# Kernel optimization log

Measured on AMD Instinct MI355X. Metric: run time of the kernel, lower is better.

The kernel has to match this reference:

```python
import jax, jax.numpy as jnp
import numpy as np

P = 16        # patch size
SIM = 0.3     # similarity threshold (forward default arg `sim`)
STY_STD = 1000.0


def patchify(imgs):
    # (N,3,H,W) -> (N, h*w, p*p*3)
    N, C, H, W = imgs.shape
    h, w = H // P, W // P
    x = imgs.reshape(N, C, h, P, w, P)
    x = jnp.einsum('nchpwq->nhwpqc', x)
    return x.reshape(N, h * w, P * P * C)


def setup_inputs() -> dict:
    key = jax.random.key(0)
    k1, k2, k3, k4 = jax.random.split(key, 4)
    N, L, D = 2, 196, 768
    x = jax.random.normal(k1, (N, L + 1, D), dtype=jnp.float32)
    imgs = jax.random.normal(k2, (N, 3, 224, 224), dtype=jnp.float32)
    # torch trunc_normal_(std=1000, a=-2, b=2) == truncated normal on [-2,2]
    learnable_sty = (jax.random.truncated_normal(
        k3, -2.0 / STY_STD, 2.0 / STY_STD, (N, L, L, 1), dtype=jnp.float32) * STY_STD)
    noise = jax.random.normal(k4, (N, L, L, 1), dtype=jnp.float32)
    return {"x": x, "imgs": imgs, "learnable_sty": learnable_sty, "noise": noise}


def reference(x, imgs, learnable_sty, noise):
    imgs = patchify(imgs)                                   # (N, L, 768)
    cls_tokens, x = x[:, :1], x[:, 1:]
    N, L, D = x.shape

    # per-patch normalization (torch.var default is unbiased -> ddof=1)
    mean = imgs.mean(axis=-1, keepdims=True)
    var = jnp.var(imgs, axis=-1, keepdims=True, ddof=1)
    imgs_n = (imgs - mean) / jnp.sqrt(var + 1e-6)
    nrm = jnp.linalg.norm(imgs_n, axis=-1)                  # (N, L)
    Sim = jnp.einsum('aik,ajk->aij', imgs_n, imgs_n) / (nrm[:, :, None] * nrm[:, None, :])

    M0 = jnp.triu((Sim > SIM).astype(jnp.float32))          # (N, L, L), binary
    rows = jnp.arange(L)

    def body(i, M):
        # original loop breaks when sum == N*L; we freeze M once that holds
        done = M.sum() == N * L
        mask = (M[:, i, :] == 0).astype(M.dtype)            # (N, L)
        # rows <= i unchanged (M*M == M for binary), rows > i masked
        upd = jnp.where(rows[None, :, None] > i, M * mask[:, None, :], M)
        return jnp.where(done, M, upd)

    M = jax.lax.fori_loop(0, L - 1, body, M0)

    # decompose: phase (con) keeps grad, amplitude (sty) is detached
    fft = jnp.fft.fftn(x, axes=(-1,))
    con, sty = jnp.angle(fft), jnp.abs(fft)
    sty_d = jax.lax.stop_gradient(sty)

    avg_sum = (M[..., None] * sty_d[:, None, :, :]).sum(axis=2)   # (N, L, D)
    sty_mask = (avg_sum > 0).astype(jnp.float32)                   # (N, L, D)
    num = M.sum(axis=2)[..., None]                                 # (N, L, 1)
    avg = avg_sum / jnp.clip(num, 1e-7, None)                      # (N, L, D)
    std = jnp.sqrt(
        (M[..., None] * (sty_d[:, None, :, :] - avg[:, :, None, :]) ** 2).sum(axis=2)
        / jnp.clip(num, 1e-7, None))                               # (N, L, D)

    sty_para = sty_mask[:, None, :, :] * learnable_sty             # (N, L, L, D)
    sty_para = sty_para / jnp.clip(sty_para.sum(axis=2, keepdims=True), 1e-7, None)
    various = noise * std[:, None, :, :] + avg[:, None, :, :]      # (N, L, L, D)
    sum_sty = (sty_para * various).sum(axis=2)                     # (N, L, D)

    # compose: ifft(amp * e^{i phase}), torch .float() keeps the real part
    out = jnp.real(jnp.fft.ifftn(sum_sty * jnp.exp(1j * con), axes=(-1,))).astype(jnp.float32)
    return jnp.concatenate((cls_tokens, out), axis=1)
```

## Files before the change

### kernel.cpp

```cpp
#include <hip/hip_runtime.h>
#include <math.h>

typedef unsigned long long u64;

#define NBATCH 2
#define LTOK 196
#define DDIM 768
#define NROWS (NBATCH*LTOK)
#define NLD (NBATCH*LTOK*DDIM)

#ifndef M_PI
#define M_PI 3.14159265358979323846
#endif
#define PI_F 3.14159265358979323846f

#define S3 0.86602540378443864676f

__device__ __forceinline__ void fft_butterfly(float* re, float* im,
                                              const float2* T,
                                              int tau, int s, int half) {
  int sub = tau >> 7;
  int b = tau & 127;
  int j = b & (half - 1);
  int p0 = (sub << 8) + ((b >> (s - 1)) << s) + j;
  int p1 = p0 + half;
  float2 w = T[j << (8 - s)];
  float xr = re[p1], xi = im[p1];
  float tr = w.x * xr - w.y * xi;
  float ti = w.x * xi + w.y * xr;
  float ur = re[p0], ui = im[p0];
  re[p0] = ur + tr; im[p0] = ui + ti;
  re[p1] = ur - tr; im[p1] = ui - ti;
}

__device__ __forceinline__ void fft_stages(float* re, float* im,
                                           const float2* T, int t) {
#pragma unroll
  for (int s = 1; s <= 8; s++) {
    int half = 1 << (s - 1);
    fft_butterfly(re, im, T, t, s, half);
    if (t < 128) fft_butterfly(re, im, T, t + 256, s, half);
    __syncthreads();
  }
}

__global__ __launch_bounds__(256) void k_pre(const float* __restrict__ imgs,
                                             const float* __restrict__ x,
                                             float* __restrict__ uT,
                                             float* __restrict__ sty,
                                             float* __restrict__ phre,
                                             float* __restrict__ phim) {
  int t = threadIdx.x;
  if (blockIdx.x < NROWS) {
    int blk = blockIdx.x;
    int a = blk / LTOK, l = blk - a * LTOK;
    int hh = l / 14, ww = l - hh * 14;
    float loc[3];
    double s = 0.0, sq = 0.0;
#pragma unroll
    for (int e = 0; e < 3; e++) {
      int d = t + (e << 8);
      int p = d / 48, r = d - p * 48;
      int q2 = r / 3, c = r - q2 * 3;
      float val = imgs[((size_t)(a * 3 + c) * 224 + (hh * 16 + p)) * 224 + (ww * 16 + q2)];
      loc[e] = val;
      s += (double)val;
      sq += (double)val * (double)val;
    }
#pragma unroll
    for (int o = 32; o > 0; o >>= 1) { s += __shfl_down(s, o); sq += __shfl_down(sq, o); }
    __shared__ double rs[4], rq[4];
    __shared__ float sh_mu, sh_sc;
    if ((t & 63) == 0) { rs[t >> 6] = s; rq[t >> 6] = sq; }
    __syncthreads();
    if (t == 0) {
      double S = rs[0] + rs[1] + rs[2] + rs[3];
      double Q = rq[0] + rq[1] + rq[2] + rq[3];
      double mean = S / 768.0;
      double ss = Q - S * S / 768.0;
      if (ss < 1e-30) ss = 1e-30;
      sh_mu = (float)mean;
      sh_sc = (float)(1.0 / sqrt(ss));
    }
    __syncthreads();
    float mu = sh_mu, sc = sh_sc;
    int col = a * LTOK + l;
#pragma unroll
    for (int e = 0; e < 3; e++) {
      int d = t + (e << 8);
      uT[(size_t)d * NROWS + col] = (loc[e] - mu) * sc;
    }
  } else {
    int blk = blockIdx.x - NROWS;
    int a = blk / LTOK, i = blk - a * LTOK;
    __shared__ float re[768], im[768];
    __shared__ float2 t256[128];
    if (t < 128) {
      float sn, cs;
      __sincosf(-2.0f * PI_F * (float)t / 256.0f, &sn, &cs);
      t256[t] = make_float2(cs, sn);
    }
    size_t row = ((size_t)a * (LTOK + 1) + 1 + i) * DDIM;
#pragma unroll
    for (int e = 0; e < 3; e++) {
      int d = t + (e << 8);
      int m = d / 3, r = d - 3 * m;
      int p = (r << 8) + (__brev((unsigned)m) >> 24);
      re[p] = x[row + d];
      im[p] = 0.f;
    }
    __syncthreads();
    fft_stages(re, im, t256, t);
    float a0r = re[t],       a0i = im[t];
    float a1r = re[256 + t], a1i = im[256 + t];
    float a2r = re[512 + t], a2i = im[512 + t];
    float sn, cs;
    __sincosf(-2.0f * PI_F * (float)t / 768.0f, &sn, &cs);
    float2 w1 = make_float2(cs, sn);
    float2 w2 = make_float2(cs * cs - sn * sn, 2.f * cs * sn);
    float b1r = a1r * w1.x - a1i * w1.y, b1i = a1r * w1.y + a1i * w1.x;
    float b2r = a2r * w2.x - a2i * w2.y, b2i = a2r * w2.y + a2i * w2.x;
    float Xr[3], Xi[3];
    Xr[0] = a0r + b1r + b2r;
    Xi[0] = a0i + b1i + b2i;
    Xr[1] = a0r + (-0.5f * b1r + S3 * b1i) + (-0.5f * b2r - S3 * b2i);
    Xi[1] = a0i + (-0.5f * b1i - S3 * b1r) + (-0.5f * b2i + S3 * b2r);
    Xr[2] = a0r + (-0.5f * b1r - S3 * b1i) + (-0.5f * b2r + S3 * b2i);
    Xi[2] = a0i + (-0.5f * b1i + S3 * b1r) + (-0.5f * b2i - S3 * b2r);
    size_t ob = ((size_t)a * LTOK + i) * DDIM + t;
#pragma unroll
    for (int s = 0; s < 3; s++) {
      float mag = sqrtf(Xr[s] * Xr[s] + Xi[s] * Xi[s]);
      size_t o = ob + (s << 8);
      sty[o] = mag;
      if (mag > 0.f) { phre[o] = Xr[s] / mag; phim[o] = Xi[s] / mag; }
      else           { phre[o] = 1.f;         phim[o] = 0.f;         }
    }
  }
}

__global__ __launch_bounds__(256) void k_sim(const float* __restrict__ uT,
                                             u64* __restrict__ Mb) {
  int blk = blockIdx.x;
  int a = blk / LTOK, i = blk - a * LTOK;
  __shared__ float ui[768];
  __shared__ u64 mask[4];
  int t = threadIdx.x;
  if (t < 4) mask[t] = 0ull;
  int coli = a * LTOK + i;
#pragma unroll
  for (int e = 0; e < 3; e++) {
    int d = t + (e << 8);
    ui[d] = uT[(size_t)d * NROWS + coli];
  }
  __syncthreads();
  int j = i + t;
  if (j < LTOK) {
    const float* col = uT + (a * LTOK + j);
    float dot = 0.f;
#pragma unroll 8
    for (int d = 0; d < 768; d++) dot += ui[d] * col[(size_t)d * NROWS];
    if (dot > 0.3f) atomicOr(&mask[j >> 6], 1ull << (j & 63));
  }
  __syncthreads();
  if (t < 4) Mb[((size_t)a * LTOK + i) * 4 + t] = mask[t];
}

__global__ __launch_bounds__(256) void k_greedy(u64* __restrict__ Mb) {
  __shared__ u64 Ml[NROWS * 4];
  __shared__ int red[4];
  __shared__ int Sdone;
  int t = threadIdx.x;
  for (int w = t; w < NROWS * 4; w += 256) Ml[w] = Mb[w];
  __syncthreads();
  for (int i = 0; i < LTOK - 1; i++) {
    int s = 0;
    for (int w = t; w < NROWS * 4; w += 256) s += __popcll(Ml[w]);
#pragma unroll
    for (int o = 32; o > 0; o >>= 1) s += __shfl_down(s, o);
    if ((t & 63) == 0) red[t >> 6] = s;
    __syncthreads();
    if (t == 0) Sdone = ((red[0] + red[1] + red[2] + red[3]) == NROWS) ? 1 : 0;
    __syncthreads();
    if (Sdone) break;
    for (int w = t; w < NROWS * 4; w += 256) {
      int a = w / (LTOK * 4);
      int rem = w - a * (LTOK * 4);
      int r = rem >> 2, wi = rem & 3;
      if (r > i) Ml[w] &= ~Ml[(a * LTOK + i) * 4 + wi];
    }
    __syncthreads();
  }
  for (int w = t; w < NROWS * 4; w += 256) Mb[w] = Ml[w];
}

__global__ __launch_bounds__(256) void k_stats(const u64* __restrict__ Mb,
                                               const float* __restrict__ sty,
                                               float* __restrict__ savg,
                                               float* __restrict__ sstd,
                                               float* __restrict__ smsk) {
  int blk = blockIdx.x;
  int a = blk / LTOK, i = blk - a * LTOK;
  __shared__ u64 mrow[4];
  int t = threadIdx.x;
  if (t < 4) mrow[t] = Mb[((size_t)a * LTOK + i) * 4 + t];
  __syncthreads();
  int num = __popcll(mrow[0]) + __popcll(mrow[1]) + __popcll(mrow[2]) + __popcll(mrow[3]);
  float fnum = fmaxf((float)num, 1e-7f);
  float acc0 = 0.f, acc1 = 0.f, acc2 = 0.f;
  for (int w = 0; w < 4; w++) {
    u64 m = mrow[w];
    while (m) {
      int b = __ffsll(m) - 1; m &= (m - 1);
      int j = (w << 6) + b;
      const float* sr = sty + ((size_t)a * LTOK + j) * DDIM;
      acc0 += sr[t]; acc1 += sr[t + 256]; acc2 += sr[t + 512];
    }
  }
  float av0 = acc0 / fnum, av1 = acc1 / fnum, av2 = acc2 / fnum;
  float sq0 = 0.f, sq1 = 0.f, sq2 = 0.f;
  for (int w = 0; w < 4; w++) {
    u64 m = mrow[w];
    while (m) {
      int b = __ffsll(m) - 1; m &= (m - 1);
      int j = (w << 6) + b;
      const float* sr = sty + ((size_t)a * LTOK + j) * DDIM;
      float d0 = sr[t] - av0, d1 = sr[t + 256] - av1, d2 = sr[t + 512] - av2;
      sq0 += d0 * d0; sq1 += d1 * d1; sq2 += d2 * d2;
    }
  }
  size_t o = ((size_t)a * LTOK + i) * DDIM + t;
  float mk0 = acc0 > 0.f ? 1.f : 0.f;
  float mk1 = acc1 > 0.f ? 1.f : 0.f;
  float mk2 = acc2 > 0.f ? 1.f : 0.f;
  smsk[o] = mk0;            smsk[o + 256] = mk1;            smsk[o + 512] = mk2;
  savg[o] = mk0 * av0;      savg[o + 256] = mk1 * av1;      savg[o + 512] = mk2 * av2;
  sstd[o] = mk0 * sqrtf(sq0 / fnum);
  sstd[o + 256] = mk1 * sqrtf(sq1 / fnum);
  sstd[o + 512] = mk2 * sqrtf(sq2 / fnum);
}

#define RTILE 7
__global__ __launch_bounds__(256) void k_combine(const float* __restrict__ ls,
                                                 const float* __restrict__ nz,
                                                 const float* __restrict__ savg,
                                                 const float* __restrict__ sstd,
                                                 const float* __restrict__ smsk,
                                                 float* __restrict__ ssum) {
  int blk = blockIdx.x;
  int a = blk / 84;
  int rem = blk - a * 84;
  int it = rem / 3, dc = rem - it * 3;
  int i0 = it * RTILE;
  int t = threadIdx.x;
  int d = (dc << 8) + t;
  __shared__ float lsr[RTILE][LTOK], lnr[RTILE][LTOK];
  for (int idx = t; idx < RTILE * LTOK; idx += 256) {
    int ii = idx / LTOK, j = idx - ii * LTOK;
    size_t o = ((size_t)(a * LTOK + i0 + ii)) * LTOK + j;
    float l = ls[o];
    lsr[ii][j] = l;
    lnr[ii][j] = l * nz[o];
  }
  __syncthreads();
  float a1[RTILE], a2[RTILE], dn[RTILE];
#pragma unroll
  for (int ii = 0; ii < RTILE; ii++) { a1[ii] = 0.f; a2[ii] = 0.f; dn[ii] = 0.f; }
#pragma unroll 2
  for (int j = 0; j < LTOK; j++) {
    size_t b = ((size_t)a * LTOK + j) * DDIM + d;
    float sd = sstd[b], sv = savg[b], sm = smsk[b];
#pragma unroll
    for (int ii = 0; ii < RTILE; ii++) {
      a1[ii] += lnr[ii][j] * sd;
      a2[ii] += lsr[ii][j] * sv;
      dn[ii] += lsr[ii][j] * sm;
    }
  }
#pragma unroll
  for (int ii = 0; ii < RTILE; ii++) {
    size_t o = ((size_t)(a * LTOK + i0 + ii)) * DDIM + d;
    ssum[o] = (a1[ii] + a2[ii]) / fmaxf(dn[ii], 1e-7f);
  }
}

__global__ __launch_bounds__(256) void k_ifft(const float* __restrict__ x,
                                              const float* __restrict__ ssum,
                                              const float* __restrict__ phre,
                                              const float* __restrict__ phim,
                                              float* __restrict__ out) {
  int blk = blockIdx.x;
  int t = threadIdx.x;
  if (blk < NBATCH) {
    size_t b = (size_t)blk * (LTOK + 1) * DDIM;
    out[b + t] = x[b + t];
    out[b + t + 256] = x[b + t + 256];
    out[b + t + 512] = x[b + t + 512];
    return;
  }
  int rr = blk - NBATCH;
  int a = rr / LTOK, i = rr - a * LTOK;
  __shared__ float re[768], im[768];
  __shared__ float2 t256[128];
  if (t < 128) {
    float sn, cs;
    __sincosf(2.0f * PI_F * (float)t / 256.0f, &sn, &cs);
    t256[t] = make_float2(cs, sn);
  }
  size_t rowz = ((size_t)a * LTOK + i) * DDIM;
#pragma unroll
  for (int e = 0; e < 3; e++) {
    int d = t + (e << 8);
    int m = d / 3, r = d - 3 * m;
    int p = (r << 8) + (__brev((unsigned)m) >> 24);
    float mg = ssum[rowz + d];
    re[p] = mg * phre[rowz + d];
    im[p] = mg * phim[rowz + d];
  }
  __syncthreads();
  fft_stages(re, im, t256, t);
  float a0r = re[t],       a0i = im[t];
  float a1r = re[256 + t], a1i = im[256 + t];
  float a2r = re[512 + t], a2i = im[512 + t];
  float sn, cs;
  __sincosf(2.0f * PI_F * (float)t / 768.0f, &sn, &cs);
  float2 w1 = make_float2(cs, sn);
  float2 w2 = make_float2(cs * cs - sn * sn, 2.f * cs * sn);
  float b1r = a1r * w1.x - a1i * w1.y, b1i = a1r * w1.y + a1i * w1.x;
  float b2r = a2r * w2.x - a2i * w2.y, b2i = a2r * w2.y + a2i * w2.x;
  float Xr[3];
  Xr[0] = a0r + b1r + b2r;
  Xr[1] = a0r + (-0.5f * b1r - S3 * b1i) + (-0.5f * b2r + S3 * b2i);
  Xr[2] = a0r + (-0.5f * b1r + S3 * b1i) + (-0.5f * b2r - S3 * b2i);
  size_t ob = ((size_t)a * (LTOK + 1) + 1 + i) * DDIM + t;
  const float inv = 1.0f / 768.0f;
  out[ob]       = Xr[0] * inv;
  out[ob + 256] = Xr[1] * inv;
  out[ob + 512] = Xr[2] * inv;
}

extern "C" void kernel_launch(void* const* d_in, const int* in_sizes, int n_in,
                              void* d_out, int out_size, void* d_ws, size_t ws_size,
                              hipStream_t stream) {
  (void)in_sizes; (void)n_in; (void)out_size; (void)ws_size;
  const float* x    = (const float*)d_in[0];
  const float* imgs = (const float*)d_in[1];
  const float* ls   = (const float*)d_in[2];
  const float* nz   = (const float*)d_in[3];
  float* out = (float*)d_out;

  float* wf   = (float*)d_ws;
  float* uT   = wf;
  float* sty  = wf + (size_t)NLD;
  float* phre = wf + 2 * (size_t)NLD;
  float* phim = wf + 3 * (size_t)NLD;
  float* sstd = wf + 4 * (size_t)NLD;
  float* smsk = wf + 5 * (size_t)NLD;
  u64* Mb = (u64*)(wf + 6 * (size_t)NLD);

  k_pre    <<<2 * NROWS, 256, 0, stream>>>(imgs, x, uT, sty, phre, phim);
  k_sim    <<<NROWS, 256, 0, stream>>>(uT, Mb);
  k_greedy <<<1, 256, 0, stream>>>(Mb);
  k_stats  <<<NROWS, 256, 0, stream>>>(Mb, sty, uT , sstd, smsk);
  k_combine<<<NBATCH * 28 * 3, 256, 0, stream>>>(ls, nz, uT , sstd, smsk, sty );
  k_ifft   <<<NBATCH + NROWS, 256, 0, stream>>>(x, sty , phre, phim, out);
}
```

Measured before the change: 145.5 us.

## Split combine reduction over j into four chunks, reduce partials in ifft

The combine kernel's loop over the 196 source tokens is split into four chunks of 49, which raises the block count from 168 to 672 so the GPU's compute units are better filled. Partial numerators and denominators are written to new workspace buffers, and the ifft kernel sums the four partials before dividing. This adds extra global writes and reads of partial sums and a larger workspace footprint in exchange for more parallelism. The two numerator accumulators are also merged into one.

Result: faster. 125.4 us (-13.8%).

```diff
diff --git a/kernel.cpp b/kernel.cpp
--- a/kernel.cpp
+++ b/kernel.cpp
@@ -9,11 +9,7 @@
 #define NROWS (NBATCH*LTOK)
 #define NLD (NBATCH*LTOK*DDIM)
 
-#ifndef M_PI
-#define M_PI 3.14159265358979323846
-#endif
 #define PI_F 3.14159265358979323846f
-
 #define S3 0.86602540378443864676f
 
 __device__ __forceinline__ void fft_butterfly(float* re, float* im,
@@ -241,51 +237,60 @@
 }
 
 #define RTILE 7
-__global__ __launch_bounds__(256) void k_combine(const float* __restrict__ ls,
-                                                 const float* __restrict__ nz,
-                                                 const float* __restrict__ savg,
-                                                 const float* __restrict__ sstd,
-                                                 const float* __restrict__ smsk,
-                                                 float* __restrict__ ssum) {
+#define JCH 4
+#define JLEN 49
+__global__ __launch_bounds__(256) void k_combine_part(const float* __restrict__ ls,
+                                                      const float* __restrict__ nz,
+                                                      const float* __restrict__ savg,
+                                                      const float* __restrict__ sstd,
+                                                      const float* __restrict__ smsk,
+                                                      float* __restrict__ numP,
+                                                      float* __restrict__ denP) {
   int blk = blockIdx.x;
-  int a = blk / 84;
-  int rem = blk - a * 84;
-  int it = rem / 3, dc = rem - it * 3;
+  int a = blk / 336;
+  int rem = blk - a * 336;
+  int it = rem / 12;
+  int r2 = rem - it * 12;
+  int dc = r2 >> 2;
+  int jc = r2 & 3;
   int i0 = it * RTILE;
+  int j0 = jc * JLEN;
   int t = threadIdx.x;
   int d = (dc << 8) + t;
-  __shared__ float lsr[RTILE][LTOK], lnr[RTILE][LTOK];
-  for (int idx = t; idx < RTILE * LTOK; idx += 256) {
-    int ii = idx / LTOK, j = idx - ii * LTOK;
-    size_t o = ((size_t)(a * LTOK + i0 + ii)) * LTOK + j;
+  __shared__ float lsr[RTILE][JLEN], lnr[RTILE][JLEN];
+  for (int idx = t; idx < RTILE * JLEN; idx += 256) {
+    int ii = idx / JLEN, j = idx - ii * JLEN;
+    size_t o = ((size_t)(a * LTOK + i0 + ii)) * LTOK + j0 + j;
     float l = ls[o];
     lsr[ii][j] = l;
     lnr[ii][j] = l * nz[o];
   }
   __syncthreads();
-  float a1[RTILE], a2[RTILE], dn[RTILE];
-#pragma unroll
-  for (int ii = 0; ii < RTILE; ii++) { a1[ii] = 0.f; a2[ii] = 0.f; dn[ii] = 0.f; }
-#pragma unroll 2
-  for (int j = 0; j < LTOK; j++) {
-    size_t b = ((size_t)a * LTOK + j) * DDIM + d;
+  float nm[RTILE], dn[RTILE];
+#pragma unroll
+  for (int ii = 0; ii < RTILE; ii++) { nm[ii] = 0.f; dn[ii] = 0.f; }
+#pragma unroll 7
+  for (int j = 0; j < JLEN; j++) {
+    size_t b = ((size_t)(a * LTOK + j0 + j)) * DDIM + d;
     float sd = sstd[b], sv = savg[b], sm = smsk[b];
 #pragma unroll
     for (int ii = 0; ii < RTILE; ii++) {
-      a1[ii] += lnr[ii][j] * sd;
-      a2[ii] += lsr[ii][j] * sv;
+      nm[ii] += lnr[ii][j] * sd;
+      nm[ii] += lsr[ii][j] * sv;
       dn[ii] += lsr[ii][j] * sm;
     }
   }
 #pragma unroll
   for (int ii = 0; ii < RTILE; ii++) {
-    size_t o = ((size_t)(a * LTOK + i0 + ii)) * DDIM + d;
-    ssum[o] = (a1[ii] + a2[ii]) / fmaxf(dn[ii], 1e-7f);
+    size_t o = ((size_t)jc * NROWS + (a * LTOK + i0 + ii)) * DDIM + d;
+    numP[o] = nm[ii];
+    denP[o] = dn[ii];
   }
 }
 
 __global__ __launch_bounds__(256) void k_ifft(const float* __restrict__ x,
-                                              const float* __restrict__ ssum,
+                                              const float* __restrict__ numP,
+                                              const float* __restrict__ denP,
                                               const float* __restrict__ phre,
                                               const float* __restrict__ phim,
                                               float* __restrict__ out) {
@@ -311,9 +316,16 @@
 #pragma unroll
   for (int e = 0; e < 3; e++) {
     int d = t + (e << 8);
+    float num = 0.f, den = 0.f;
+#pragma unroll
+    for (int jc = 0; jc < JCH; jc++) {
+      size_t o = (size_t)jc * NROWS * DDIM + rowz + d;
+      num += numP[o];
+      den += denP[o];
+    }
+    float mg = num / fmaxf(den, 1e-7f);
     int m = d / 3, r = d - 3 * m;
     int p = (r << 8) + (__brev((unsigned)m) >> 24);
-    float mg = ssum[rowz + d];
     re[p] = mg * phre[rowz + d];
     im[p] = mg * phim[rowz + d];
   }
@@ -356,12 +368,14 @@
   float* phim = wf + 3 * (size_t)NLD;
   float* sstd = wf + 4 * (size_t)NLD;
   float* smsk = wf + 5 * (size_t)NLD;
-  u64* Mb = (u64*)(wf + 6 * (size_t)NLD);
-
-  k_pre    <<<2 * NROWS, 256, 0, stream>>>(imgs, x, uT, sty, phre, phim);
-  k_sim    <<<NROWS, 256, 0, stream>>>(uT, Mb);
-  k_greedy <<<1, 256, 0, stream>>>(Mb);
-  k_stats  <<<NROWS, 256, 0, stream>>>(Mb, sty, uT , sstd, smsk);
-  k_combine<<<NBATCH * 28 * 3, 256, 0, stream>>>(ls, nz, uT , sstd, smsk, sty );
-  k_ifft   <<<NBATCH + NROWS, 256, 0, stream>>>(x, sty , phre, phim, out);
-}
+  float* numP = wf + 6 * (size_t)NLD;
+  float* denP = wf + 10 * (size_t)NLD;
+  u64* Mb = (u64*)(wf + 14 * (size_t)NLD);
+
+  k_pre         <<<2 * NROWS, 256, 0, stream>>>(imgs, x, uT, sty, phre, phim);
+  k_sim         <<<NROWS, 256, 0, stream>>>(uT, Mb);
+  k_greedy      <<<1, 256, 0, stream>>>(Mb);
+  k_stats       <<<NROWS, 256, 0, stream>>>(Mb, sty, uT , sstd, smsk);
+  k_combine_part<<<NBATCH * 28 * 3 * JCH, 256, 0, stream>>>(ls, nz, uT , sstd, smsk, numP, denP);
+  k_ifft        <<<NBATCH + NROWS, 256, 0, stream>>>(x, numP, denP, phre, phim, out);
+}
```
